# Optimization experiments

Hardware: AMD Instinct MI355X
Metric: run time of the kernel (lower is better)

## Reference

```python
import jax, jax.numpy as jnp
import numpy as np

N = 8192
D = 64
NEG = -9.0e15  # matches torch's -9000000000000000.0 mask value


def _xavier_bound(fan_in, fan_out, gain):
    return gain * np.sqrt(6.0 / (fan_in + fan_out))


def setup_inputs() -> dict:
    key = jax.random.key(0)
    k1, k2, k3 = jax.random.split(key, 3)
    x = jax.random.normal(k1, (N, D), dtype=jnp.float32)
    gain = np.sqrt(2.0)  # calculate_gain('relu')
    b = _xavier_bound(2 * D, 1, gain)
    A1 = jax.random.uniform(k2, (2 * D, 1), dtype=jnp.float32, minval=-b, maxval=b)
    A2 = jax.random.uniform(k3, (2 * D, 1), dtype=jnp.float32, minval=-b, maxval=b)
    return {"x": x, "A1": A1, "A2": A2}


def _adj_mask(n):
    # adj = eye(n); adj[:,0]=1; adj[0,:]=1  -> star graph + self loops
    m = jnp.eye(n, dtype=bool)
    m = m.at[:, 0].set(True)
    m = m.at[0, :].set(True)
    return m


def _gat_layer(h, A, d):
    h1 = h @ A[d:, :]            # [n,1]
    h2 = h @ A[:d, :]            # [n,1]
    e = h1 + h2.T                # [n,n] broadcasted score matrix
    mask = _adj_mask(h.shape[0])
    att = jax.nn.softmax(jnp.where(mask, e, NEG), axis=-1)  # [n,n]
    return att @ h               # [n,d]


def reference(x, A1, A2):
    d = x.shape[1]
    x1 = _gat_layer(x, A1, d)    # in2hidden
    x2 = _gat_layer(x1, A2, d)   # hidden2out
    return x2
```

## Files before the change

kernel.cpp:

```cpp
#include <hip/hip_runtime.h>
#include <math.h>

#define NROWS 8192
#define DD    64
#define K1B   256
#define K1T   512
#define K1W   8
#define K1RPW (NROWS / (K1B * K1W))
#define K2B   256
#define K2T   512


__device__ __forceinline__ float wsum64(float v) {
    #pragma unroll
    for (int o = 32; o; o >>= 1) v += __shfl_xor(v, o);
    return v;
}

__global__ __launch_bounds__(K1T) void gat_k1(
    const float* __restrict__ x, const float* __restrict__ A1,
    const float* __restrict__ A2, float* __restrict__ out,
    float* __restrict__ e2, float* __restrict__ part1, float* __restrict__ z1,
    float* __restrict__ part2, float* __restrict__ z2)
{
    const int lane = threadIdx.x & 63;
    const int wl   = threadIdx.x >> 6;
    const int r0   = (blockIdx.x * K1W + wl) * K1RPW;

    __shared__ float sa[K1W][DD], sb[K1W][DD];
    __shared__ float sza[K1W], szb[K1W];

    float w1 = A1[lane], w2 = A2[lane];
    float x0 = x[lane];
    float e10 = expf(wsum64(x0 * w1));

    float a1 = 0.f, q1 = 0.f, a2 = 0.f, q2 = 0.f;
    #pragma unroll
    for (int k = 0; k < K1RPW; ++k) {
        int r = r0 + k;
        float hv = x[r * DD + lane];
        float e1 = expf(wsum64(hv * w1));
        a1 += e1 * hv;
        q1 += e1;
        if (r != 0) {
            float o1 = (e10 * x0 + e1 * hv) / (e10 + e1);
            out[r * DD + lane] = o1;
            float e2r = expf(wsum64(o1 * w2));
            if (lane == 0) e2[r] = e2r;
            a2 += e2r * o1;
            q2 += e2r;
        }
    }
    sa[wl][lane] = a1; sb[wl][lane] = a2;
    if (lane == 0) { sza[wl] = q1; szb[wl] = q2; }
    __syncthreads();
    if (wl == 0) {
        float p1 = 0.f, p2 = 0.f;
        #pragma unroll
        for (int j = 0; j < K1W; ++j) { p1 += sa[j][lane]; p2 += sb[j][lane]; }
        part1[blockIdx.x * DD + lane] = p1;
        part2[blockIdx.x * DD + lane] = p2;
        if (lane == 0) {
            float u1 = 0.f, u2 = 0.f;
            #pragma unroll
            for (int j = 0; j < K1W; ++j) { u1 += sza[j]; u2 += szb[j]; }
            z1[blockIdx.x] = u1; z2[blockIdx.x] = u2;
        }
    }
}

__global__ __launch_bounds__(K2T) void gat_k2(
    const float* __restrict__ A2, float* __restrict__ out,
    const float* __restrict__ e2,
    const float* __restrict__ part1, const float* __restrict__ z1,
    const float* __restrict__ part2, const float* __restrict__ z2)
{
    const int tid  = threadIdx.x;
    const int lane = tid & 63;
    const int wl   = tid >> 6;
    const int cg   = lane & 15;
    const int grp  = lane >> 4;
    const int row  = blockIdx.x * 32 + (tid >> 4);

    float4 hv4 = *(const float4*)(out + row * DD + cg * 4);
    float  er  = e2[row];

    __shared__ float4 swa[8][16];
    __shared__ float  szw[8];
    __shared__ float4 h0sh[16];
    __shared__ float  e20sh;
    __shared__ float4 out0sh[16];

    {
        const float4* P = (const float4*)part1;
        int p0 = wl * 32 + grp;
        float4 s = make_float4(0.f, 0.f, 0.f, 0.f);
        float zs = 0.f;
        #pragma unroll
        for (int i = 0; i < 8; ++i) {
            float4 v = P[(p0 + i * 4) * 16 + cg];
            s.x += v.x; s.y += v.y; s.z += v.z; s.w += v.w;
            zs += z1[p0 + i * 4];
        }
        #pragma unroll
        for (int o = 16; o <= 32; o <<= 1) {
            s.x += __shfl_xor(s.x, o); s.y += __shfl_xor(s.y, o);
            s.z += __shfl_xor(s.z, o); s.w += __shfl_xor(s.w, o);
            zs  += __shfl_xor(zs, o);
        }
        if (lane < 16) swa[wl][lane] = s;
        if (lane == 0) szw[wl] = zs;
    }
    __syncthreads();
    if (wl == 0 && lane < 16) {
        float4 h = swa[0][lane];
        #pragma unroll
        for (int j = 1; j < 8; ++j) {
            float4 v = swa[j][lane];
            h.x += v.x; h.y += v.y; h.z += v.z; h.w += v.w;
        }
        float Z = 0.f;
        #pragma unroll
        for (int j = 0; j < 8; ++j) Z += szw[j];
        float inv = 1.f / Z;
        float4 h0 = make_float4(h.x * inv, h.y * inv, h.z * inv, h.w * inv);
        h0sh[lane] = h0;
        float4 a24 = ((const float4*)A2)[lane];
        float d = h0.x * a24.x + h0.y * a24.y + h0.z * a24.z + h0.w * a24.w;
        #pragma unroll
        for (int o = 8; o; o >>= 1) d += __shfl_xor(d, o);
        if (lane == 0) e20sh = expf(d);
    }
    __syncthreads();

    if (blockIdx.x == 0) {
        const float4* P = (const float4*)part2;
        int p0 = wl * 32 + grp;
        float4 s = make_float4(0.f, 0.f, 0.f, 0.f);
        float zs = 0.f;
        #pragma unroll
        for (int i = 0; i < 8; ++i) {
            float4 v = P[(p0 + i * 4) * 16 + cg];
            s.x += v.x; s.y += v.y; s.z += v.z; s.w += v.w;
            zs += z2[p0 + i * 4];
        }
        #pragma unroll
        for (int o = 16; o <= 32; o <<= 1) {
            s.x += __shfl_xor(s.x, o); s.y += __shfl_xor(s.y, o);
            s.z += __shfl_xor(s.z, o); s.w += __shfl_xor(s.w, o);
            zs  += __shfl_xor(zs, o);
        }
        if (lane < 16) swa[wl][lane] = s;
        if (lane == 0) szw[wl] = zs;
    }
    __syncthreads();
    if (blockIdx.x == 0 && wl == 0 && lane < 16) {
        float4 p = swa[0][lane];
        #pragma unroll
        for (int j = 1; j < 8; ++j) {
            float4 v = swa[j][lane];
            p.x += v.x; p.y += v.y; p.z += v.z; p.w += v.w;
        }
        float Zb = 0.f;
        #pragma unroll
        for (int j = 0; j < 8; ++j) Zb += szw[j];
        float e20 = e20sh;
        float4 h0 = h0sh[lane];
        float inv = 1.f / (Zb + e20);
        out0sh[lane] = make_float4((p.x + e20 * h0.x) * inv,
                                   (p.y + e20 * h0.y) * inv,
                                   (p.z + e20 * h0.z) * inv,
                                   (p.w + e20 * h0.w) * inv);
    }
    __syncthreads();

    float  e20 = e20sh;
    float4 h0  = h0sh[cg];
    float4 o4;
    if (row == 0) {
        o4 = out0sh[cg];
    } else {
        float inv = 1.f / (e20 + er);
        o4 = make_float4((e20 * h0.x + er * hv4.x) * inv,
                         (e20 * h0.y + er * hv4.y) * inv,
                         (e20 * h0.z + er * hv4.z) * inv,
                         (e20 * h0.w + er * hv4.w) * inv);
    }
    *(float4*)(out + row * DD + cg * 4) = o4;
}

extern "C" void kernel_launch(void* const* d_in, const int* in_sizes, int n_in,
                              void* d_out, int out_size, void* d_ws, size_t ws_size,
                              hipStream_t stream)
{
    const float* x  = (const float*)d_in[0];
    const float* A1 = (const float*)d_in[1];
    const float* A2 = (const float*)d_in[2];
    float* out = (float*)d_out;
    float* ws  = (float*)d_ws;

    float* part1 = ws;
    float* z1    = part1 + K1B * DD;
    float* part2 = z1 + K1B;
    float* z2    = part2 + K1B * DD;
    float* e2    = z2 + K1B;

    gat_k1<<<K1B, K1T, 0, stream>>>(x, A1, A2, out, e2, part1, z1, part2, z2);
    gat_k2<<<K2B, K2T, 0, stream>>>(A2, out, e2, part1, z1, part2, z2);
}
```

Baseline: 14.47 us.

## Recompute layer-1 rows in second kernel instead of storing intermediates

The first kernel no longer writes the per-row layer-1 output and its exp score to global memory. The second kernel instead reloads x and recomputes each non-hub row's layer-1 result and layer-2 score with 16-lane shuffle reductions. The first kernel also drops to 128 blocks, so each wave handles more rows and the partial-sum reduction in the second kernel reads fewer entries. This cuts a full N×D intermediate write and re-read, at the price of extra exps and shuffles in the second kernel.

```diff
diff --git a/kernel.cpp b/kernel.cpp
--- a/kernel.cpp
+++ b/kernel.cpp
@@ -3,7 +3,7 @@
 
 #define NROWS 8192
 #define DD    64
-#define K1B   256
+#define K1B   128
 #define K1T   512
 #define K1W   8
 #define K1RPW (NROWS / (K1B * K1W))
@@ -19,8 +19,8 @@
 
 __global__ __launch_bounds__(K1T) void gat_k1(
     const float* __restrict__ x, const float* __restrict__ A1,
-    const float* __restrict__ A2, float* __restrict__ out,
-    float* __restrict__ e2, float* __restrict__ part1, float* __restrict__ z1,
+    const float* __restrict__ A2,
+    float* __restrict__ part1, float* __restrict__ z1,
     float* __restrict__ part2, float* __restrict__ z2)
 {
     const int lane = threadIdx.x & 63;
@@ -44,9 +44,7 @@
         q1 += e1;
         if (r != 0) {
             float o1 = (e10 * x0 + e1 * hv) / (e10 + e1);
-            out[r * DD + lane] = o1;
             float e2r = expf(wsum64(o1 * w2));
-            if (lane == 0) e2[r] = e2r;
             a2 += e2r * o1;
             q2 += e2r;
         }
@@ -70,8 +68,8 @@
 }
 
 __global__ __launch_bounds__(K2T) void gat_k2(
+    const float* __restrict__ x, const float* __restrict__ A1,
     const float* __restrict__ A2, float* __restrict__ out,
-    const float* __restrict__ e2,
     const float* __restrict__ part1, const float* __restrict__ z1,
     const float* __restrict__ part2, const float* __restrict__ z2)
 {
@@ -82,8 +80,10 @@
     const int grp  = lane >> 4;
     const int row  = blockIdx.x * 32 + (tid >> 4);
 
-    float4 hv4 = *(const float4*)(out + row * DD + cg * 4);
-    float  er  = e2[row];
+    float4 xrf = *(const float4*)(x + row * DD + cg * 4);
+    float4 x0f = ((const float4*)x)[cg];
+    float4 w1f = ((const float4*)A1)[cg];
+    float4 w2f = ((const float4*)A2)[cg];
 
     __shared__ float4 swa[8][16];
     __shared__ float  szw[8];
@@ -93,11 +93,11 @@
 
     {
         const float4* P = (const float4*)part1;
-        int p0 = wl * 32 + grp;
+        int p0 = wl * 16 + grp;
         float4 s = make_float4(0.f, 0.f, 0.f, 0.f);
         float zs = 0.f;
         #pragma unroll
-        for (int i = 0; i < 8; ++i) {
+        for (int i = 0; i < 4; ++i) {
             float4 v = P[(p0 + i * 4) * 16 + cg];
             s.x += v.x; s.y += v.y; s.z += v.z; s.w += v.w;
             zs += z1[p0 + i * 4];
@@ -135,11 +135,11 @@
 
     if (blockIdx.x == 0) {
         const float4* P = (const float4*)part2;
-        int p0 = wl * 32 + grp;
+        int p0 = wl * 16 + grp;
         float4 s = make_float4(0.f, 0.f, 0.f, 0.f);
         float zs = 0.f;
         #pragma unroll
-        for (int i = 0; i < 8; ++i) {
+        for (int i = 0; i < 4; ++i) {
             float4 v = P[(p0 + i * 4) * 16 + cg];
             s.x += v.x; s.y += v.y; s.z += v.z; s.w += v.w;
             zs += z2[p0 + i * 4];
@@ -180,11 +180,25 @@
     if (row == 0) {
         o4 = out0sh[cg];
     } else {
-        float inv = 1.f / (e20 + er);
-        o4 = make_float4((e20 * h0.x + er * hv4.x) * inv,
-                         (e20 * h0.y + er * hv4.y) * inv,
-                         (e20 * h0.z + er * hv4.z) * inv,
-                         (e20 * h0.w + er * hv4.w) * inv);
+        float s0 = x0f.x * w1f.x + x0f.y * w1f.y + x0f.z * w1f.z + x0f.w * w1f.w;
+        float sr = xrf.x * w1f.x + xrf.y * w1f.y + xrf.z * w1f.z + xrf.w * w1f.w;
+        #pragma unroll
+        for (int o = 8; o; o >>= 1) { s0 += __shfl_xor(s0, o); sr += __shfl_xor(sr, o); }
+        float e10 = expf(s0), e1 = expf(sr);
+        float i1 = 1.f / (e10 + e1);
+        float4 h1 = make_float4((e10 * x0f.x + e1 * xrf.x) * i1,
+                                (e10 * x0f.y + e1 * xrf.y) * i1,
+                                (e10 * x0f.z + e1 * xrf.z) * i1,
+                                (e10 * x0f.w + e1 * xrf.w) * i1);
+        float tr = h1.x * w2f.x + h1.y * w2f.y + h1.z * w2f.z + h1.w * w2f.w;
+        #pragma unroll
+        for (int o = 8; o; o >>= 1) tr += __shfl_xor(tr, o);
+        float e2 = expf(tr);
+        float i2 = 1.f / (e20 + e2);
+        o4 = make_float4((e20 * h0.x + e2 * h1.x) * i2,
+                         (e20 * h0.y + e2 * h1.y) * i2,
+                         (e20 * h0.z + e2 * h1.z) * i2,
+                         (e20 * h0.w + e2 * h1.w) * i2);
     }
     *(float4*)(out + row * DD + cg * 4) = o4;
 }
@@ -203,8 +217,7 @@
     float* z1    = part1 + K1B * DD;
     float* part2 = z1 + K1B;
     float* z2    = part2 + K1B * DD;
-    float* e2    = z2 + K1B;
-
-    gat_k1<<<K1B, K1T, 0, stream>>>(x, A1, A2, out, e2, part1, z1, part2, z2);
-    gat_k2<<<K2B, K2T, 0, stream>>>(A2, out, e2, part1, z1, part2, z2);
-}
+
+    gat_k1<<<K1B, K1T, 0, stream>>>(x, A1, A2, part1, z1, part2, z2);
+    gat_k2<<<K2B, K2T, 0, stream>>>(x, A1, A2, out, part1, z1, part2, z2);
+}
```

Result: faster. 14.08 us, median of 2 (-2.7%).
